# Performance work log

Hardware: AMD Instinct MI355X
Metric: run time of the kernel (lower is better)

## Reference

```python
import jax, jax.numpy as jnp
import numpy as np

N_NODES = 50000
N_EDGES = 800000
D_IN = 100
HID = 128
N_LAYERS = 3
N_GRAPHS = 64


def setup_inputs() -> dict:
    key = jax.random.key(0)
    ks = jax.random.split(key, 10)
    x = jax.random.normal(ks[0], (N_NODES, D_IN), dtype=jnp.float32)
    edge_index = jax.random.randint(ks[1], (2, N_EDGES), 0, N_NODES, dtype=jnp.int64)
    batch = jnp.sort(jax.random.randint(ks[2], (N_NODES,), 0, N_GRAPHS, dtype=jnp.int64))
    s = 1.0 / np.sqrt(D_IN)
    W_enc = jax.random.uniform(ks[3], (D_IN, HID), jnp.float32, -s, s)
    b_enc = jax.random.uniform(ks[4], (HID,), jnp.float32, -s, s)
    sh = 1.0 / np.sqrt(HID)
    gcn_W = jax.random.uniform(ks[5], (N_LAYERS, HID, HID), jnp.float32, -sh, sh)
    gcn_b = jax.random.uniform(ks[6], (N_LAYERS, HID), jnp.float32, -sh, sh)
    W_reg = jax.random.uniform(ks[7], (HID, 1), jnp.float32, -sh, sh)
    b_reg = jax.random.uniform(ks[8], (1,), jnp.float32, -sh, sh)
    return {"x": x, "edge_index": edge_index, "batch": batch,
            "W_enc": W_enc, "b_enc": b_enc, "gcn_W": gcn_W, "gcn_b": gcn_b,
            "W_reg": W_reg, "b_reg": b_reg}


def reference(x, edge_index, batch, W_enc, b_enc, gcn_W, gcn_b, W_reg, b_reg):
    N = x.shape[0]
    # node encoder
    h = x @ W_enc + b_enc  # [N, HID]
    # GCN normalization with self-loops (edge_weight = 1, PyG gcn_norm)
    loop = jnp.arange(N, dtype=edge_index.dtype)
    src = jnp.concatenate([edge_index[0], loop])  # [E+N]
    dst = jnp.concatenate([edge_index[1], loop])
    deg = jax.ops.segment_sum(jnp.ones_like(src, dtype=h.dtype), dst, num_segments=N)
    dinv = jnp.where(deg > 0, jax.lax.rsqrt(deg), 0.0)
    norm = dinv[src] * dinv[dst]  # [E+N]
    for i in range(N_LAYERS):
        m = (h @ gcn_W[i])[src] * norm[:, None]           # gather + scale messages
        h = jax.ops.segment_sum(m, dst, num_segments=N)   # scatter-add aggregate
        h = jax.nn.relu(h + gcn_b[i])
    # global mean pool over graphs
    sums = jax.ops.segment_sum(h, batch, num_segments=N_GRAPHS)
    cnt = jax.ops.segment_sum(jnp.ones((N,), dtype=h.dtype), batch, num_segments=N_GRAPHS)
    pooled = sums / jnp.maximum(cnt, 1.0)[:, None]        # [N_GRAPHS, HID]
    return pooled @ W_reg + b_reg                         # [N_GRAPHS, 1]
```

## Files before the change

### kernel.cpp

```cpp
#include <hip/hip_runtime.h>
#include <hip/hip_fp16.h>

#define N_NODES 50000
#define N_EDGES 800000
#define D_INN 100
#define HID 128
#define N_GRAPHS 64
#define NBLK ((N_NODES + 255) / 256)
#define POOL_ROWS 128
#define POOL_BLOCKS ((N_NODES + POOL_ROWS - 1) / POOL_ROWS)

#define NBUCK 8
#define NODES_PER_BUCK (N_NODES / NBUCK)
#define SCAT_BLOCKS 2048

typedef _Float16 f16x8 __attribute__((ext_vector_type(8)));
typedef float f32x4 __attribute__((ext_vector_type(4)));

__global__ void k_init(int* __restrict__ deg, float* __restrict__ sums) {
    int i = blockIdx.x * 256 + threadIdx.x;
    if (i < N_NODES) deg[i] = 1;
    if (i < N_GRAPHS * HID) sums[i] = 0.f;
}

__global__ __launch_bounds__(256) void k_deg(const int* __restrict__ dst,
                                             int* __restrict__ deg) {
    int b = blockIdx.x & (NBUCK - 1);
    int lo = b * NODES_PER_BUCK, hi = lo + NODES_PER_BUCK;
    int sub = blockIdx.x >> 3, nsub = gridDim.x >> 3;
    for (int e = sub * 256 + threadIdx.x; e < N_EDGES; e += nsub * 256) {
        int d = dst[e];
        if (d >= lo && d < hi) atomicAdd(&deg[d], 1);
    }
}

__global__ __launch_bounds__(256) void k_scan1(const int* __restrict__ deg,
                                               int* __restrict__ incl,
                                               int* __restrict__ bsums) {
    __shared__ int sm[256];
    int i = blockIdx.x * 256 + threadIdx.x;
    int v = (i < N_NODES) ? deg[i] : 0;
    sm[threadIdx.x] = v;
    __syncthreads();
    for (int off = 1; off < 256; off <<= 1) {
        int t = (threadIdx.x >= off) ? sm[threadIdx.x - off] : 0;
        __syncthreads();
        sm[threadIdx.x] += t;
        __syncthreads();
    }
    if (i < N_NODES) incl[i] = sm[threadIdx.x];
    if (threadIdx.x == 255) bsums[blockIdx.x] = sm[255];
}

__global__ __launch_bounds__(256) void k_scan2(const int* __restrict__ bsums,
                                               int* __restrict__ boff) {
    __shared__ int sm[256];
    int v = (threadIdx.x < NBLK) ? bsums[threadIdx.x] : 0;
    sm[threadIdx.x] = v;
    __syncthreads();
    for (int off = 1; off < 256; off <<= 1) {
        int t = (threadIdx.x >= off) ? sm[threadIdx.x - off] : 0;
        __syncthreads();
        sm[threadIdx.x] += t;
        __syncthreads();
    }
    boff[threadIdx.x] = sm[threadIdx.x] - v;
}

__global__ void k_scan3(const int* __restrict__ incl, const int* __restrict__ boff,
                        const int* __restrict__ deg, int* __restrict__ offsets,
                        int* __restrict__ cursor, int* __restrict__ csr_src,
                        float* __restrict__ dinv) {
    int i = blockIdx.x * 256 + threadIdx.x;
    if (i < N_NODES) {
        int off1 = incl[i] + boff[blockIdx.x];
        offsets[i + 1] = off1;
        int dg = deg[i];
        int p0 = off1 - dg;
        csr_src[p0] = i;
        cursor[i] = p0 + 1;
        dinv[i] = rsqrtf((float)dg);
    }
    if (i == 0) offsets[0] = 0;
}

__global__ __launch_bounds__(256) void k_fill(const int* __restrict__ src,
                                              const int* __restrict__ dst,
                                              int* __restrict__ cursor,
                                              int* __restrict__ csr_src) {
    int b = blockIdx.x & (NBUCK - 1);
    int lo = b * NODES_PER_BUCK, hi = lo + NODES_PER_BUCK;
    int sub = blockIdx.x >> 3, nsub = gridDim.x >> 3;
    for (int e = sub * 256 + threadIdx.x; e < N_EDGES; e += nsub * 256) {
        int d = dst[e];
        if (d >= lo && d < hi) {
            int s = src[e];
            int p = atomicAdd(&cursor[d], 1);
            csr_src[p] = s;
        }
    }
}

__global__ void k_wts(const float* __restrict__ W, const float* __restrict__ We,
                      __half* __restrict__ Wt, __half* __restrict__ Wte) {
    int i = blockIdx.x * 256 + threadIdx.x;
    if (i < 3 * HID * HID) {
        int l = i >> 14, rem = i & 16383;
        int c = rem >> 7, k = rem & 127;
        Wt[(l << 14) + c * HID + k] = __float2half(W[(l << 14) + k * HID + c]);
    } else if (i < 4 * HID * HID) {
        int j = i - 3 * HID * HID;
        int c = j >> 7, k = j & 127;
        float v = (k < D_INN) ? We[k * HID + c] : 0.f;
        Wte[c * HID + k] = __float2half(v);
    }
}

__global__ void k_xh(const float* __restrict__ x, __half2* __restrict__ xh) {
    int i = blockIdx.x * 256 + threadIdx.x;
    if (i < N_NODES * 64) {
        int r = i >> 6, c = (i & 63) * 2;
        float v0 = (c     < D_INN) ? x[r * D_INN + c]     : 0.f;
        float v1 = (c + 1 < D_INN) ? x[r * D_INN + c + 1] : 0.f;
        xh[i] = __floats2half2_rn(v0, v1);
    }
}

template <bool BIAS, bool DINV>
__global__ __launch_bounds__(256) void k_gemm_mfma(const _Float16* __restrict__ A,
                                                   const _Float16* __restrict__ Wt,
                                                   const float* __restrict__ bias,
                                                   const float* __restrict__ dinv,
                                                   _Float16* __restrict__ out) {
    const int lane = threadIdx.x & 63;
    const int wave = threadIdx.x >> 6;
    const int l15  = lane & 15;
    const int lhi  = lane >> 4;
    f16x8 bf0[4], bf1[4];
#pragma unroll
    for (int ks = 0; ks < 4; ++ks) {
        int col0 = wave * 32 + l15;
        int col1 = wave * 32 + 16 + l15;
        bf0[ks] = *(const f16x8*)(Wt + col0 * HID + ks * 32 + lhi * 8);
        bf1[ks] = *(const f16x8*)(Wt + col1 * HID + ks * 32 + lhi * 8);
    }
    float b0 = 0.f, b1 = 0.f;
    if (BIAS) {
        b0 = bias[wave * 32 + l15];
        b1 = bias[wave * 32 + 16 + l15];
    }
    for (int chunk = blockIdx.x; chunk < N_NODES / 16; chunk += gridDim.x) {
        int row0 = chunk * 16;
        const _Float16* Ar = A + (row0 + l15) * HID + lhi * 8;
        f16x8 af0 = *(const f16x8*)(Ar);
        f16x8 af1 = *(const f16x8*)(Ar + 32);
        f16x8 af2 = *(const f16x8*)(Ar + 64);
        f16x8 af3 = *(const f16x8*)(Ar + 96);
        f32x4 acc0 = {0.f, 0.f, 0.f, 0.f};
        f32x4 acc1 = {0.f, 0.f, 0.f, 0.f};
        acc0 = __builtin_amdgcn_mfma_f32_16x16x32_f16(af0, bf0[0], acc0, 0, 0, 0);
        acc1 = __builtin_amdgcn_mfma_f32_16x16x32_f16(af0, bf1[0], acc1, 0, 0, 0);
        acc0 = __builtin_amdgcn_mfma_f32_16x16x32_f16(af1, bf0[1], acc0, 0, 0, 0);
        acc1 = __builtin_amdgcn_mfma_f32_16x16x32_f16(af1, bf1[1], acc1, 0, 0, 0);
        acc0 = __builtin_amdgcn_mfma_f32_16x16x32_f16(af2, bf0[2], acc0, 0, 0, 0);
        acc1 = __builtin_amdgcn_mfma_f32_16x16x32_f16(af2, bf1[2], acc1, 0, 0, 0);
        acc0 = __builtin_amdgcn_mfma_f32_16x16x32_f16(af3, bf0[3], acc0, 0, 0, 0);
        acc1 = __builtin_amdgcn_mfma_f32_16x16x32_f16(af3, bf1[3], acc1, 0, 0, 0);
#pragma unroll
        for (int r = 0; r < 4; ++r) {
            int row = row0 + lhi * 4 + r;
            float v0 = acc0[r] + b0;
            float v1 = acc1[r] + b1;
            if (DINV) {
                float dr = dinv[row];
                v0 *= dr; v1 *= dr;
            }
            out[row * HID + wave * 32 + l15]      = (_Float16)v0;
            out[row * HID + wave * 32 + 16 + l15] = (_Float16)v1;
        }
    }
}

__global__ __launch_bounds__(256) void k_agg(const __half* __restrict__ B,
                                             const int* __restrict__ offsets,
                                             const int* __restrict__ csr_src,
                                             const float* __restrict__ dinv,
                                             const float* __restrict__ bias,
                                             __half* __restrict__ A) {
    int node = (blockIdx.x * 256 + threadIdx.x) >> 6;
    int lane = threadIdx.x & 63;
    if (node >= N_NODES) return;
    int beg = offsets[node], end = offsets[node + 1];
    float ax0 = 0.f, ay0 = 0.f, ax1 = 0.f, ay1 = 0.f;
    const __half2* B2 = (const __half2*)B;
    int j = beg;
    while (j < end) {
        int take = end - j; if (take > 64) take = 64;
        int s_l = (lane < take) ? csr_src[j + lane] : 0;
        int t = 0;
        for (; t + 8 <= take; t += 8) {
            int s0 = __shfl(s_l, t + 0), s1 = __shfl(s_l, t + 1);
            int s2 = __shfl(s_l, t + 2), s3 = __shfl(s_l, t + 3);
            int s4 = __shfl(s_l, t + 4), s5 = __shfl(s_l, t + 5);
            int s6 = __shfl(s_l, t + 6), s7 = __shfl(s_l, t + 7);
            __half2 v0 = B2[s0 * 64 + lane];
            __half2 v1 = B2[s1 * 64 + lane];
            __half2 v2 = B2[s2 * 64 + lane];
            __half2 v3 = B2[s3 * 64 + lane];
            __half2 v4 = B2[s4 * 64 + lane];
            __half2 v5 = B2[s5 * 64 + lane];
            __half2 v6 = B2[s6 * 64 + lane];
            __half2 v7 = B2[s7 * 64 + lane];
            float2 f0 = __half22float2(v0);
            float2 f1 = __half22float2(v1);
            float2 f2 = __half22float2(v2);
            float2 f3 = __half22float2(v3);
            float2 f4 = __half22float2(v4);
            float2 f5 = __half22float2(v5);
            float2 f6 = __half22float2(v6);
            float2 f7 = __half22float2(v7);
            ax0 += f0.x; ay0 += f0.y;
            ax1 += f1.x; ay1 += f1.y;
            ax0 += f2.x; ay0 += f2.y;
            ax1 += f3.x; ay1 += f3.y;
            ax0 += f4.x; ay0 += f4.y;
            ax1 += f5.x; ay1 += f5.y;
            ax0 += f6.x; ay0 += f6.y;
            ax1 += f7.x; ay1 += f7.y;
        }
        for (; t + 4 <= take; t += 4) {
            int s0 = __shfl(s_l, t + 0), s1 = __shfl(s_l, t + 1);
            int s2 = __shfl(s_l, t + 2), s3 = __shfl(s_l, t + 3);
            float2 f0 = __half22float2(B2[s0 * 64 + lane]);
            float2 f1 = __half22float2(B2[s1 * 64 + lane]);
            float2 f2 = __half22float2(B2[s2 * 64 + lane]);
            float2 f3 = __half22float2(B2[s3 * 64 + lane]);
            ax0 += f0.x; ay0 += f0.y;
            ax1 += f1.x; ay1 += f1.y;
            ax0 += f2.x; ay0 += f2.y;
            ax1 += f3.x; ay1 += f3.y;
        }
        for (; t < take; ++t) {
            int s = __shfl(s_l, t);
            float2 f = __half22float2(B2[s * 64 + lane]);
            ax0 += f.x; ay0 += f.y;
        }
        j += take;
    }
    float dn = dinv[node];
    float2 b = ((const float2*)bias)[lane];
    float rx = fmaxf(fmaf(dn, ax0 + ax1, b.x), 0.f);
    float ry = fmaxf(fmaf(dn, ay0 + ay1, b.y), 0.f);
    ((__half2*)A)[node * 64 + lane] = __floats2half2_rn(rx, ry);
}

__global__ __launch_bounds__(64) void k_pool_part(const __half* __restrict__ A,
                                                  const int* __restrict__ batch,
                                                  float* __restrict__ sums) {
    int base = blockIdx.x * POOL_ROWS;
    if (base >= N_NODES) return;
    int c = threadIdx.x;
    int end = base + POOL_ROWS;
    if (end > N_NODES) end = N_NODES;
    const __half2* A2 = (const __half2*)A;
    float ax = 0.f, ay = 0.f;
    int g = batch[base];
    for (int n = base; n < end; ++n) {
        int bg = batch[n];
        if (bg != g) {
            atomicAdd(&sums[g * HID + 2 * c], ax);
            atomicAdd(&sums[g * HID + 2 * c + 1], ay);
            ax = 0.f; ay = 0.f;
            g = bg;
        }
        float2 f = __half22float2(A2[n * 64 + c]);
        ax += f.x; ay += f.y;
    }
    atomicAdd(&sums[g * HID + 2 * c], ax);
    atomicAdd(&sums[g * HID + 2 * c + 1], ay);
}

__global__ __launch_bounds__(128) void k_head(const float* __restrict__ sums,
                                              const int* __restrict__ batch,
                                              const float* __restrict__ W_reg,
                                              const float* __restrict__ b_reg,
                                              float* __restrict__ out) {
    int g = blockIdx.x;
    int lo = 0, hi = N_NODES;
    while (lo < hi) { int mid = (lo + hi) >> 1; if (batch[mid] < g) lo = mid + 1; else hi = mid; }
    int start = lo;
    hi = N_NODES;
    while (lo < hi) { int mid = (lo + hi) >> 1; if (batch[mid] < g + 1) lo = mid + 1; else hi = mid; }
    int end = lo;
    float cnt = (float)((end - start) > 0 ? (end - start) : 1);
    float v = (sums[g * HID + threadIdx.x] / cnt) * W_reg[threadIdx.x];
    for (int off = 32; off > 0; off >>= 1) v += __shfl_down(v, off);
    __shared__ float sm[2];
    if ((threadIdx.x & 63) == 0) sm[threadIdx.x >> 6] = v;
    __syncthreads();
    if (threadIdx.x == 0) out[g] = sm[0] + sm[1] + b_reg[0];
}

extern "C" void kernel_launch(void* const* d_in, const int* in_sizes, int n_in,
                              void* d_out, int out_size, void* d_ws, size_t ws_size,
                              hipStream_t stream) {
    const float* x      = (const float*)d_in[0];
    const int*   e_src  = (const int*)d_in[1];
    const int*   e_dst  = e_src + N_EDGES;
    const int*   batch  = (const int*)d_in[2];
    const float* W_enc  = (const float*)d_in[3];
    const float* b_enc  = (const float*)d_in[4];
    const float* gcn_W  = (const float*)d_in[5];
    const float* gcn_b  = (const float*)d_in[6];
    const float* W_reg  = (const float*)d_in[7];
    const float* b_reg  = (const float*)d_in[8];
    float* out = (float*)d_out;

    char* p = (char*)d_ws;
    auto carve = [&](size_t bytes) { char* q = p; p += (bytes + 255) & ~(size_t)255; return q; };
    __half* hA      = (__half*)carve(sizeof(__half) * N_NODES * HID);
    __half* msg     = (__half*)carve(sizeof(__half) * N_NODES * HID);
    __half* xh      = (__half*)carve(sizeof(__half) * N_NODES * HID);
    __half* Wt      = (__half*)carve(sizeof(__half) * 3 * HID * HID);
    __half* Wte     = (__half*)carve(sizeof(__half) * HID * HID);
    int*    csr_src = (int*)   carve(sizeof(int)    * (N_EDGES + N_NODES));
    int*    deg     = (int*)   carve(sizeof(int)    * N_NODES);
    int*    cursor  = (int*)   carve(sizeof(int)    * N_NODES);
    int*    offsets = (int*)   carve(sizeof(int)    * (N_NODES + 1));
    int*    incl    = (int*)   carve(sizeof(int)    * N_NODES);
    int*    bsums   = (int*)   carve(sizeof(int)    * 256);
    int*    boff    = (int*)   carve(sizeof(int)    * 256);
    float*  dinv    = (float*) carve(sizeof(float)  * N_NODES);
    float*  sums    = (float*) carve(sizeof(float)  * N_GRAPHS * HID);

    k_init<<<NBLK, 256, 0, stream>>>(deg, sums);
    k_deg<<<SCAT_BLOCKS, 256, 0, stream>>>(e_dst, deg);
    k_scan1<<<NBLK, 256, 0, stream>>>(deg, incl, bsums);
    k_scan2<<<1, 256, 0, stream>>>(bsums, boff);
    k_scan3<<<NBLK, 256, 0, stream>>>(incl, boff, deg, offsets, cursor, csr_src, dinv);
    k_fill<<<SCAT_BLOCKS, 256, 0, stream>>>(e_src, e_dst, cursor, csr_src);

    k_wts<<<(4 * HID * HID + 255) / 256, 256, 0, stream>>>(gcn_W, W_enc, Wt, Wte);
    k_xh<<<(N_NODES * 64 + 255) / 256, 256, 0, stream>>>(x, (__half2*)xh);

    k_gemm_mfma<true, false><<<640, 256, 0, stream>>>(
        (const _Float16*)xh, (const _Float16*)Wte, b_enc, nullptr, (_Float16*)hA);
    for (int l = 0; l < 3; ++l) {
        k_gemm_mfma<false, true><<<640, 256, 0, stream>>>(
            (const _Float16*)hA, (const _Float16*)(Wt + l * HID * HID), nullptr, dinv,
            (_Float16*)msg);
        k_agg<<<(N_NODES * 64 + 255) / 256, 256, 0, stream>>>(
            msg, offsets, csr_src, dinv, gcn_b + l * HID, hA);
    }
    k_pool_part<<<POOL_BLOCKS, 64, 0, stream>>>(hA, batch, sums);
    k_head<<<N_GRAPHS, 128, 0, stream>>>(sums, batch, W_reg, b_reg, out);
}
```

Before: 369.7 us.

## Fuse x fp16 conversion into encoder GEMM and vectorize transposed MFMA stores

The separate x-to-fp16 kernel and its intermediate buffer are removed. The encoder GEMM now reads the fp32 input directly and converts it in registers. The MFMA operands are swapped so that each lane holds four consecutive output features of one node, which lets the GEMMs write f16x4 stores instead of scattered scalar half stores. The weight-transpose kernel is also merged into the init kernel, and the GEMM grid is changed from 640 to 512 blocks. The aim is to cut a full memory pass, two launches and store inefficiency, at the cost of unaligned-tail handling for the 100-wide input rows.

```diff
diff --git a/kernel.cpp b/kernel.cpp
--- a/kernel.cpp
+++ b/kernel.cpp
@@ -13,14 +13,32 @@
 #define NBUCK 8
 #define NODES_PER_BUCK (N_NODES / NBUCK)
 #define SCAT_BLOCKS 2048
+#define GEMM_BLOCKS 512
+#define N_CHUNK (N_NODES / 16)
 
 typedef _Float16 f16x8 __attribute__((ext_vector_type(8)));
+typedef _Float16 f16x4 __attribute__((ext_vector_type(4)));
 typedef float f32x4 __attribute__((ext_vector_type(4)));
 
-__global__ void k_init(int* __restrict__ deg, float* __restrict__ sums) {
+__global__ __launch_bounds__(256) void k_setup(int* __restrict__ deg,
+                                               float* __restrict__ sums,
+                                               const float* __restrict__ W,
+                                               const float* __restrict__ We,
+                                               __half* __restrict__ Wt,
+                                               __half* __restrict__ Wte) {
     int i = blockIdx.x * 256 + threadIdx.x;
     if (i < N_NODES) deg[i] = 1;
     if (i < N_GRAPHS * HID) sums[i] = 0.f;
+    if (i < 3 * HID * HID) {
+        int l = i >> 14, rem = i & 16383;
+        int c = rem >> 7, k = rem & 127;
+        Wt[(l << 14) + c * HID + k] = __float2half(W[(l << 14) + k * HID + c]);
+    } else if (i < 4 * HID * HID) {
+        int j = i - 3 * HID * HID;
+        int c = j >> 7, k = j & 127;
+        float v = (k < D_INN) ? We[k * HID + c] : 0.f;
+        Wte[c * HID + k] = __float2half(v);
+    }
 }
 
 __global__ __launch_bounds__(256) void k_deg(const int* __restrict__ dst,
@@ -101,83 +119,105 @@
     }
 }
 
-__global__ void k_wts(const float* __restrict__ W, const float* __restrict__ We,
-                      __half* __restrict__ Wt, __half* __restrict__ Wte) {
-    int i = blockIdx.x * 256 + threadIdx.x;
-    if (i < 3 * HID * HID) {
-        int l = i >> 14, rem = i & 16383;
-        int c = rem >> 7, k = rem & 127;
-        Wt[(l << 14) + c * HID + k] = __float2half(W[(l << 14) + k * HID + c]);
-    } else if (i < 4 * HID * HID) {
-        int j = i - 3 * HID * HID;
-        int c = j >> 7, k = j & 127;
-        float v = (k < D_INN) ? We[k * HID + c] : 0.f;
-        Wte[c * HID + k] = __float2half(v);
-    }
-}
-
-__global__ void k_xh(const float* __restrict__ x, __half2* __restrict__ xh) {
-    int i = blockIdx.x * 256 + threadIdx.x;
-    if (i < N_NODES * 64) {
-        int r = i >> 6, c = (i & 63) * 2;
-        float v0 = (c     < D_INN) ? x[r * D_INN + c]     : 0.f;
-        float v1 = (c + 1 < D_INN) ? x[r * D_INN + c + 1] : 0.f;
-        xh[i] = __floats2half2_rn(v0, v1);
-    }
-}
-
-template <bool BIAS, bool DINV>
-__global__ __launch_bounds__(256) void k_gemm_mfma(const _Float16* __restrict__ A,
-                                                   const _Float16* __restrict__ Wt,
-                                                   const float* __restrict__ bias,
-                                                   const float* __restrict__ dinv,
-                                                   _Float16* __restrict__ out) {
+__global__ __launch_bounds__(256) void k_genc(const float* __restrict__ x,
+                                              const _Float16* __restrict__ Wt,
+                                              const float* __restrict__ bias,
+                                              _Float16* __restrict__ out) {
     const int lane = threadIdx.x & 63;
     const int wave = threadIdx.x >> 6;
     const int l15  = lane & 15;
     const int lhi  = lane >> 4;
-    f16x8 bf0[4], bf1[4];
+    f16x8 wf0[4], wf1[4];
 #pragma unroll
     for (int ks = 0; ks < 4; ++ks) {
-        int col0 = wave * 32 + l15;
-        int col1 = wave * 32 + 16 + l15;
-        bf0[ks] = *(const f16x8*)(Wt + col0 * HID + ks * 32 + lhi * 8);
-        bf1[ks] = *(const f16x8*)(Wt + col1 * HID + ks * 32 + lhi * 8);
-    }
-    float b0 = 0.f, b1 = 0.f;
-    if (BIAS) {
-        b0 = bias[wave * 32 + l15];
-        b1 = bias[wave * 32 + 16 + l15];
-    }
-    for (int chunk = blockIdx.x; chunk < N_NODES / 16; chunk += gridDim.x) {
+        wf0[ks] = *(const f16x8*)(Wt + (wave * 32 + l15) * HID + ks * 32 + lhi * 8);
+        wf1[ks] = *(const f16x8*)(Wt + (wave * 32 + 16 + l15) * HID + ks * 32 + lhi * 8);
+    }
+    f32x4 bq0 = ((const f32x4*)bias)[wave * 8 + lhi];
+    f32x4 bq1 = ((const f32x4*)bias)[wave * 8 + 4 + lhi];
+    for (int chunk = blockIdx.x; chunk < N_CHUNK; chunk += gridDim.x) {
+        int row0 = chunk * 16;
+        const float* xr = x + (row0 + l15) * D_INN + lhi * 8;
+        f16x8 nf[4];
+#pragma unroll
+        for (int ks = 0; ks < 3; ++ks) {
+            float4 a = *(const float4*)(xr + ks * 32);
+            float4 b = *(const float4*)(xr + ks * 32 + 4);
+            f16x8 t;
+            t[0] = (_Float16)a.x; t[1] = (_Float16)a.y;
+            t[2] = (_Float16)a.z; t[3] = (_Float16)a.w;
+            t[4] = (_Float16)b.x; t[5] = (_Float16)b.y;
+            t[6] = (_Float16)b.z; t[7] = (_Float16)b.w;
+            nf[ks] = t;
+        }
+        {
+            f16x8 t;
+            int kb = 96 + lhi * 8;
+#pragma unroll
+            for (int j = 0; j < 8; ++j)
+                t[j] = (kb + j < D_INN) ? (_Float16)xr[96 + j] : (_Float16)0.f;
+            nf[3] = t;
+        }
+        f32x4 acc0 = {0.f, 0.f, 0.f, 0.f};
+        f32x4 acc1 = {0.f, 0.f, 0.f, 0.f};
+#pragma unroll
+        for (int ks = 0; ks < 4; ++ks) {
+            acc0 = __builtin_amdgcn_mfma_f32_16x16x32_f16(wf0[ks], nf[ks], acc0, 0, 0, 0);
+            acc1 = __builtin_amdgcn_mfma_f32_16x16x32_f16(wf1[ks], nf[ks], acc1, 0, 0, 0);
+        }
+        int node = row0 + l15;
+        f16x4 o0, o1;
+#pragma unroll
+        for (int r = 0; r < 4; ++r) {
+            o0[r] = (_Float16)(acc0[r] + bq0[r]);
+            o1[r] = (_Float16)(acc1[r] + bq1[r]);
+        }
+        *(f16x4*)(out + node * HID + wave * 32 + lhi * 4) = o0;
+        *(f16x4*)(out + node * HID + wave * 32 + 16 + lhi * 4) = o1;
+    }
+}
+
+__global__ __launch_bounds__(256) void k_gemm(const _Float16* __restrict__ A,
+                                              const _Float16* __restrict__ Wt,
+                                              const float* __restrict__ dinv,
+                                              _Float16* __restrict__ out) {
+    const int lane = threadIdx.x & 63;
+    const int wave = threadIdx.x >> 6;
+    const int l15  = lane & 15;
+    const int lhi  = lane >> 4;
+    f16x8 wf0[4], wf1[4];
+#pragma unroll
+    for (int ks = 0; ks < 4; ++ks) {
+        wf0[ks] = *(const f16x8*)(Wt + (wave * 32 + l15) * HID + ks * 32 + lhi * 8);
+        wf1[ks] = *(const f16x8*)(Wt + (wave * 32 + 16 + l15) * HID + ks * 32 + lhi * 8);
+    }
+    for (int chunk = blockIdx.x; chunk < N_CHUNK; chunk += gridDim.x) {
         int row0 = chunk * 16;
         const _Float16* Ar = A + (row0 + l15) * HID + lhi * 8;
-        f16x8 af0 = *(const f16x8*)(Ar);
-        f16x8 af1 = *(const f16x8*)(Ar + 32);
-        f16x8 af2 = *(const f16x8*)(Ar + 64);
-        f16x8 af3 = *(const f16x8*)(Ar + 96);
+        f16x8 nf0 = *(const f16x8*)(Ar);
+        f16x8 nf1 = *(const f16x8*)(Ar + 32);
+        f16x8 nf2 = *(const f16x8*)(Ar + 64);
+        f16x8 nf3 = *(const f16x8*)(Ar + 96);
         f32x4 acc0 = {0.f, 0.f, 0.f, 0.f};
         f32x4 acc1 = {0.f, 0.f, 0.f, 0.f};
-        acc0 = __builtin_amdgcn_mfma_f32_16x16x32_f16(af0, bf0[0], acc0, 0, 0, 0);
-        acc1 = __builtin_amdgcn_mfma_f32_16x16x32_f16(af0, bf1[0], acc1, 0, 0, 0);
-        acc0 = __builtin_amdgcn_mfma_f32_16x16x32_f16(af1, bf0[1], acc0, 0, 0, 0);
-        acc1 = __builtin_amdgcn_mfma_f32_16x16x32_f16(af1, bf1[1], acc1, 0, 0, 0);
-        acc0 = __builtin_amdgcn_mfma_f32_16x16x32_f16(af2, bf0[2], acc0, 0, 0, 0);
-        acc1 = __builtin_amdgcn_mfma_f32_16x16x32_f16(af2, bf1[2], acc1, 0, 0, 0);
-        acc0 = __builtin_amdgcn_mfma_f32_16x16x32_f16(af3, bf0[3], acc0, 0, 0, 0);
-        acc1 = __builtin_amdgcn_mfma_f32_16x16x32_f16(af3, bf1[3], acc1, 0, 0, 0);
+        acc0 = __builtin_amdgcn_mfma_f32_16x16x32_f16(wf0[0], nf0, acc0, 0, 0, 0);
+        acc1 = __builtin_amdgcn_mfma_f32_16x16x32_f16(wf1[0], nf0, acc1, 0, 0, 0);
+        acc0 = __builtin_amdgcn_mfma_f32_16x16x32_f16(wf0[1], nf1, acc0, 0, 0, 0);
+        acc1 = __builtin_amdgcn_mfma_f32_16x16x32_f16(wf1[1], nf1, acc1, 0, 0, 0);
+        acc0 = __builtin_amdgcn_mfma_f32_16x16x32_f16(wf0[2], nf2, acc0, 0, 0, 0);
+        acc1 = __builtin_amdgcn_mfma_f32_16x16x32_f16(wf1[2], nf2, acc1, 0, 0, 0);
+        acc0 = __builtin_amdgcn_mfma_f32_16x16x32_f16(wf0[3], nf3, acc0, 0, 0, 0);
+        acc1 = __builtin_amdgcn_mfma_f32_16x16x32_f16(wf1[3], nf3, acc1, 0, 0, 0);
+        int node = row0 + l15;
+        float dr = dinv[node];
+        f16x4 o0, o1;
 #pragma unroll
         for (int r = 0; r < 4; ++r) {
-            int row = row0 + lhi * 4 + r;
-            float v0 = acc0[r] + b0;
-            float v1 = acc1[r] + b1;
-            if (DINV) {
-                float dr = dinv[row];
-                v0 *= dr; v1 *= dr;
-            }
-            out[row * HID + wave * 32 + l15]      = (_Float16)v0;
-            out[row * HID + wave * 32 + 16 + l15] = (_Float16)v1;
-        }
+            o0[r] = (_Float16)(acc0[r] * dr);
+            o1[r] = (_Float16)(acc1[r] * dr);
+        }
+        *(f16x4*)(out + node * HID + wave * 32 + lhi * 4) = o0;
+        *(f16x4*)(out + node * HID + wave * 32 + 16 + lhi * 4) = o1;
     }
 }
 
@@ -320,7 +360,6 @@
     auto carve = [&](size_t bytes) { char* q = p; p += (bytes + 255) & ~(size_t)255; return q; };
     __half* hA      = (__half*)carve(sizeof(__half) * N_NODES * HID);
     __half* msg     = (__half*)carve(sizeof(__half) * N_NODES * HID);
-    __half* xh      = (__half*)carve(sizeof(__half) * N_NODES * HID);
     __half* Wt      = (__half*)carve(sizeof(__half) * 3 * HID * HID);
     __half* Wte     = (__half*)carve(sizeof(__half) * HID * HID);
     int*    csr_src = (int*)   carve(sizeof(int)    * (N_EDGES + N_NODES));
@@ -333,21 +372,18 @@
     float*  dinv    = (float*) carve(sizeof(float)  * N_NODES);
     float*  sums    = (float*) carve(sizeof(float)  * N_GRAPHS * HID);
 
-    k_init<<<NBLK, 256, 0, stream>>>(deg, sums);
+    k_setup<<<256, 256, 0, stream>>>(deg, sums, gcn_W, W_enc, Wt, Wte);
     k_deg<<<SCAT_BLOCKS, 256, 0, stream>>>(e_dst, deg);
     k_scan1<<<NBLK, 256, 0, stream>>>(deg, incl, bsums);
     k_scan2<<<1, 256, 0, stream>>>(bsums, boff);
     k_scan3<<<NBLK, 256, 0, stream>>>(incl, boff, deg, offsets, cursor, csr_src, dinv);
     k_fill<<<SCAT_BLOCKS, 256, 0, stream>>>(e_src, e_dst, cursor, csr_src);
 
-    k_wts<<<(4 * HID * HID + 255) / 256, 256, 0, stream>>>(gcn_W, W_enc, Wt, Wte);
-    k_xh<<<(N_NODES * 64 + 255) / 256, 256, 0, stream>>>(x, (__half2*)xh);
-
-    k_gemm_mfma<true, false><<<640, 256, 0, stream>>>(
-        (const _Float16*)xh, (const _Float16*)Wte, b_enc, nullptr, (_Float16*)hA);
+    k_genc<<<GEMM_BLOCKS, 256, 0, stream>>>(
+        x, (const _Float16*)Wte, b_enc, (_Float16*)hA);
     for (int l = 0; l < 3; ++l) {
-        k_gemm_mfma<false, true><<<640, 256, 0, stream>>>(
-            (const _Float16*)hA, (const _Float16*)(Wt + l * HID * HID), nullptr, dinv,
+        k_gemm<<<GEMM_BLOCKS, 256, 0, stream>>>(
+            (const _Float16*)hA, (const _Float16*)(Wt + l * HID * HID), dinv,
             (_Float16*)msg);
         k_agg<<<(N_NODES * 64 + 255) / 256, 256, 0, stream>>>(
             msg, offsets, csr_src, dinv, gcn_b + l * HID, hA);
```

Result: faster. 360.7 us (median of 2 runs) (-2.5%).
